# Optimization experiments

Measured on AMD Instinct MI355X. Metric: run time of the kernel, lower is better.

Reference implementation:

```python
import jax, jax.numpy as jnp
import numpy as np

N = 384          # nodes per graph
HID = 128        # hid_dim
H = 8            # shared_num_heads
C = HID // H     # shared_head_dim = 16
L = 4            # num_layers
VOCAB = 20
NORB = 4
NCAT = NORB * NORB + NORB   # 20 edge categories
OUT = 10
B = 4
E = N * N        # fully-connected closure incl. self loops
EPS = 1e-5


def layer_norm(x, g, b):
    m = jnp.mean(x, axis=-1, keepdims=True)
    v = jnp.mean((x - m) ** 2, axis=-1, keepdims=True)
    return (x - m) / jnp.sqrt(v + EPS) * g + b


def setup_inputs() -> dict:
    key = jax.random.key(0)
    ks = iter(jax.random.split(key, 32))

    def nrm(shape, s=0.05):
        return jax.random.normal(next(ks), shape, jnp.float32) * s

    # edge structure: fully connected, edge (i,j) in row-major order
    pos = np.arange(N) % NORB                    # node -> orbit
    src = np.repeat(np.arange(N), N)
    tgt = np.tile(np.arange(N), N)
    cat = np.where(src == tgt, NORB * NORB + pos[src], pos[src] * NORB + pos[tgt])

    x = jax.random.randint(next(ks), (B, N, 1), 0, VOCAB, jnp.int32)

    return dict(
        x=x,
        edge_src=jnp.asarray(src, jnp.int32),
        edge_tgt=jnp.asarray(tgt, jnp.int32),
        edge_cat=jnp.asarray(cat, jnp.int32),
        token_emb=nrm((VOCAB, HID), 1.0),
        edge_emb=nrm((NCAT, HID), 1.0),
        ln_in1_g=jnp.ones((HID,), jnp.float32), ln_in1_b=jnp.zeros((HID,), jnp.float32),
        W_in=nrm((HID, HID)), b_in=jnp.zeros((HID,), jnp.float32),
        ln_in2_g=jnp.ones((HID,), jnp.float32), ln_in2_b=jnp.zeros((HID,), jnp.float32),
        Wl=nrm((L, HID, H * C)), bl=jnp.zeros((L, H * C), jnp.float32),
        Wr=nrm((L, HID, H * C)), br=jnp.zeros((L, H * C), jnp.float32),
        We=nrm((L, HID, H * C)),                           # lin_edge has no bias in PyG GATv2Conv
        att=nrm((L, H, C)),
        bias_gat=jnp.zeros((L, H * C), jnp.float32),
        W_proj=nrm((L, HID, HID)), b_proj=jnp.zeros((L, HID), jnp.float32),
        ln_g=jnp.ones((L, HID), jnp.float32), ln_b=jnp.zeros((L, HID), jnp.float32),
        W_out=nrm((HID, OUT)), b_out=jnp.zeros((OUT,), jnp.float32),
    )


def reference(x, edge_src, edge_tgt, edge_cat,
              token_emb, edge_emb,
              ln_in1_g, ln_in1_b, W_in, b_in, ln_in2_g, ln_in2_b,
              Wl, bl, Wr, br, We, att, bias_gat,
              W_proj, b_proj, ln_g, ln_b, W_out, b_out):
    edge_feat = edge_emb[edge_cat]                       # [E, HID] gather by category
    h = token_emb[x[..., 0]]                             # [B, N, HID]
    # input MLP: LN -> ReLU -> Linear -> LN
    h = layer_norm(h, ln_in1_g, ln_in1_b)
    h = jax.nn.relu(h)
    h = h @ W_in + b_in
    h = layer_norm(h, ln_in2_g, ln_in2_b)

    for l in range(L):
        edge_e = (edge_feat @ We[l]).reshape(E, H, C)    # shared across batch

        def conv(hb):  # hb: [N, HID]  GATv2Conv, concat heads
            xl = (hb @ Wl[l] + bl[l]).reshape(N, H, C)   # source transform
            xr = (hb @ Wr[l] + br[l]).reshape(N, H, C)   # target transform
            e = jax.nn.leaky_relu(xl[edge_src] + xr[edge_tgt] + edge_e, 0.2)  # [E,H,C]
            logits = jnp.einsum('ehc,hc->eh', e, att[l])                      # [E,H]
            # segment softmax over edges sharing a target node
            m = jax.ops.segment_max(logits, edge_tgt, num_segments=N)
            ex = jnp.exp(logits - m[edge_tgt])
            den = jax.ops.segment_sum(ex, edge_tgt, num_segments=N)
            alpha = ex / den[edge_tgt]                                        # [E,H]
            out = jax.ops.segment_sum(xl[edge_src] * alpha[:, :, None], edge_tgt,
                                      num_segments=N)                         # [N,H,C]
            return out.reshape(N, H * C) + bias_gat[l]

        h_prev = h
        h = jax.vmap(conv)(h)                            # [B, N, HID]
        h = h @ W_proj[l] + b_proj[l]
        h = layer_norm(h, ln_g[l], ln_b[l])
        h = jax.nn.relu(h) + h_prev                      # residual

    h = h.sum(axis=1)                                    # sum over nodes -> [B, HID]
    return h @ W_out + b_out                             # [B, OUT]
```

## Files before the change

kernel.cpp:

```cpp
#include <hip/hip_runtime.h>


#define NN 384
#define NB 4
#define TJ 3

__device__ __forceinline__ void reduce32(float& a, float& b) {
#pragma unroll
  for (int m = 1; m <= 16; m <<= 1) {
    a += __shfl_xor(a, m, 64);
    b += __shfl_xor(b, m, 64);
  }
}

__global__ __launch_bounds__(256) void k_init(
    const int* __restrict__ x,
    const float* __restrict__ token_emb, const float* __restrict__ edge_emb,
    const float* __restrict__ ln1g, const float* __restrict__ ln1b,
    const float* __restrict__ W_in, const float* __restrict__ b_in,
    const float* __restrict__ ln2g, const float* __restrict__ ln2b,
    const float* __restrict__ Wl, const float* __restrict__ bl,
    const float* __restrict__ Wr, const float* __restrict__ br,
    const float* __restrict__ We, const float* __restrict__ att_w,
    float* __restrict__ ce, float* __restrict__ h,
    float* __restrict__ xl, float* __restrict__ xr, float* __restrict__ datt0)
{
  const int blk = blockIdx.x, t = threadIdx.x;
  if (blk < 40) {
    const int idx = blk * 256 + t;
    const int hc = idx & 127, rest = idx >> 7;
    const int cat = rest % 20, l = rest / 20;
    const float* er = edge_emb + cat * 128;
    const float* w  = We + (l * 128) * 128 + hc;
    float acc = 0.f;
#pragma unroll 8
    for (int k = 0; k < 128; ++k) acc = fmaf(er[k], w[k * 128], acc);
    ce[idx] = acc;
    return;
  }
  __shared__ float trow[8][128];
  __shared__ float hbuf[8][128];
  const int r0 = (blk - 40) * 8;
  const int r = t >> 5, cw = (t & 31) * 4;
  const int row = r0 + r;
  const int tok = x[row];
  float4 v = *(const float4*)(token_emb + tok * 128 + cw);
  float s1 = v.x + v.y + v.z + v.w;
  float s2 = v.x * v.x + v.y * v.y + v.z * v.z + v.w * v.w;
  reduce32(s1, s2);
  float mean = s1 * 0.0078125f;
  float inv  = rsqrtf(s2 * 0.0078125f - mean * mean + 1e-5f);
  {
    float4 g  = *(const float4*)(ln1g + cw);
    float4 bb = *(const float4*)(ln1b + cw);
    trow[r][cw + 0] = fmaxf((v.x - mean) * inv * g.x + bb.x, 0.f);
    trow[r][cw + 1] = fmaxf((v.y - mean) * inv * g.y + bb.y, 0.f);
    trow[r][cw + 2] = fmaxf((v.z - mean) * inv * g.z + bb.z, 0.f);
    trow[r][cw + 3] = fmaxf((v.w - mean) * inv * g.w + bb.w, 0.f);
  }
  __syncthreads();
  const int o = t & 127, rh = (t >> 7) * 4;
  float a0, a1, a2, a3;
  { float bo = b_in[o]; a0 = a1 = a2 = a3 = bo; }
  for (int k = 0; k < 128; ++k) {
    float w = W_in[k * 128 + o];
    a0 = fmaf(trow[rh + 0][k], w, a0);
    a1 = fmaf(trow[rh + 1][k], w, a1);
    a2 = fmaf(trow[rh + 2][k], w, a2);
    a3 = fmaf(trow[rh + 3][k], w, a3);
  }
  hbuf[rh + 0][o] = a0; hbuf[rh + 1][o] = a1;
  hbuf[rh + 2][o] = a2; hbuf[rh + 3][o] = a3;
  __syncthreads();
  v = *(const float4*)(&hbuf[r][cw]);
  s1 = v.x + v.y + v.z + v.w;
  s2 = v.x * v.x + v.y * v.y + v.z * v.z + v.w * v.w;
  reduce32(s1, s2);
  mean = s1 * 0.0078125f;
  inv  = rsqrtf(s2 * 0.0078125f - mean * mean + 1e-5f);
  {
    float4 g  = *(const float4*)(ln2g + cw);
    float4 bb = *(const float4*)(ln2b + cw);
    float4 hv;
    hv.x = (v.x - mean) * inv * g.x + bb.x;
    hv.y = (v.y - mean) * inv * g.y + bb.y;
    hv.z = (v.z - mean) * inv * g.z + bb.z;
    hv.w = (v.w - mean) * inv * g.w + bb.w;
    *(float4*)(&trow[r][cw]) = hv;
    *(float4*)(h + row * 128 + cw) = hv;
  }
  __syncthreads();
  float l0, l1, l2, l3, q0, q1, q2, q3;
  { float blo = bl[o], bro = br[o]; l0 = l1 = l2 = l3 = blo; q0 = q1 = q2 = q3 = bro; }
  for (int k = 0; k < 128; ++k) {
    float wl = Wl[k * 128 + o], wr = Wr[k * 128 + o];
    float h0 = trow[rh + 0][k], h1 = trow[rh + 1][k];
    float h2 = trow[rh + 2][k], h3 = trow[rh + 3][k];
    l0 = fmaf(h0, wl, l0); q0 = fmaf(h0, wr, q0);
    l1 = fmaf(h1, wl, l1); q1 = fmaf(h1, wr, q1);
    l2 = fmaf(h2, wl, l2); q2 = fmaf(h2, wr, q2);
    l3 = fmaf(h3, wl, l3); q3 = fmaf(h3, wr, q3);
  }
  const int rb = r0 + rh;
  xl[(rb + 0) * 128 + o] = l0; xr[(rb + 0) * 128 + o] = q0;
  xl[(rb + 1) * 128 + o] = l1; xr[(rb + 1) * 128 + o] = q1;
  xl[(rb + 2) * 128 + o] = l2; xr[(rb + 2) * 128 + o] = q2;
  xl[(rb + 3) * 128 + o] = l3; xr[(rb + 3) * 128 + o] = q3;
  {
    float av = att_w[o];
    float s0 = av * l0, sA = av * l1, sB = av * l2, sC = av * l3;
#pragma unroll
    for (int mm = 1; mm <= 8; mm <<= 1) {
      s0 += __shfl_xor(s0, mm, 64);
      sA += __shfl_xor(sA, mm, 64);
      sB += __shfl_xor(sB, mm, 64);
      sC += __shfl_xor(sC, mm, 64);
    }
    if ((t & 15) == 0) {
      const int hh2 = o >> 4;
      const int bb2 = r0 / NN, ii = r0 - bb2 * NN + rh;
      const int base = (bb2 * 8 + hh2) * NN + ii;
      datt0[base + 0] = s0; datt0[base + 1] = sA;
      datt0[base + 2] = sB; datt0[base + 3] = sC;
    }
  }
}

__global__ __launch_bounds__(256) void k_layer(
    const float* __restrict__ xl_in, const float* __restrict__ xr_in,
    const float* __restrict__ datt_in,
    float* __restrict__ xl_out, float* __restrict__ xr_out,
    float* __restrict__ datt_out,
    float* __restrict__ h, const float* __restrict__ ce,
    const float* __restrict__ att_w, const float* __restrict__ bias_gat,
    const float* __restrict__ W_proj, const float* __restrict__ b_proj,
    const float* __restrict__ ln_g, const float* __restrict__ ln_b,
    const float* __restrict__ Wl, const float* __restrict__ bl,
    const float* __restrict__ Wr, const float* __restrict__ br,
    int l, int next_l)
{
  __shared__ float xrce[TJ][5][136];
  __shared__ float djr02[TJ][5][8];
  __shared__ float mbuf[8][32][17];
  __shared__ float arow[TJ][132];
  __shared__ float pbuf[2 * TJ][132];
  __shared__ float nrow[TJ][132];

  const int blk = blockIdx.x, t = threadIdx.x;
  const int jt = blk & 127, b = blk >> 7;
  const int j0 = jt * TJ;

  for (int idx = t; idx < TJ * 5 * 128; idx += 256) {
    const int hc = idx & 127, rest = idx >> 7;
    const int sel = rest % 5, jj = rest / 5;
    const int j = j0 + jj, pj = j & 3;
    const int cat = (sel == 4) ? (16 + pj) : (sel * 4 + pj);
    xrce[jj][sel][hc] = xr_in[(b * NN + j) * 128 + hc] + ce[(l * 20 + cat) * 128 + hc];
  }
  __syncthreads();
  if (t < TJ * 5 * 8) {
    const int jj = t / 40, r2 = t % 40, sel = r2 >> 3, h2 = r2 & 7;
    float d = 0.f;
#pragma unroll
    for (int c = 0; c < 16; ++c)
      d += xrce[jj][sel][h2 * 16 + c] * att_w[l * 128 + h2 * 16 + c];
    djr02[jj][sel][h2] = 0.2f * d;
  }
  __syncthreads();

  const int hh = t >> 5, isub = t & 31;
  float attv[16];
  {
    const float* ap = att_w + l * 128 + hh * 16;
#pragma unroll
    for (int c = 0; c < 16; ++c) attv[c] = ap[c];
  }
  float sden[TJ];
  float acc[TJ][16];
#pragma unroll
  for (int jj = 0; jj < TJ; ++jj) {
    sden[jj] = 0.f;
#pragma unroll
    for (int c = 0; c < 16; ++c) acc[jj][c] = 0.f;
  }
  const float* xlb = xl_in + (b * NN) * 128 + hh * 16;
  const float* dp  = datt_in + (b * 8 + hh) * NN;

  for (int it = 0; it < NN / 32; ++it) {
    const int i = isub + 32 * it;
    float xv[16];
    {
      const float4* xp = (const float4*)(xlb + i * 128);
#pragma unroll
      for (int q = 0; q < 4; ++q) {
        float4 a = xp[q];
        xv[q * 4 + 0] = a.x; xv[q * 4 + 1] = a.y;
        xv[q * 4 + 2] = a.z; xv[q * 4 + 3] = a.w;
      }
    }
    const float di02 = 0.2f * dp[i];
    const int pi = i & 3;
#pragma unroll
    for (int jj = 0; jj < TJ; ++jj) {
      const int sel = (i == j0 + jj) ? 4 : pi;
      const float4* bp = (const float4*)(&xrce[jj][sel][hh * 16]);
      float p = 0.f;
#pragma unroll
      for (int q = 0; q < 4; ++q) {
        float4 cv = bp[q];
        p = fmaf(fmaxf(xv[q * 4 + 0] + cv.x, 0.f), attv[q * 4 + 0], p);
        p = fmaf(fmaxf(xv[q * 4 + 1] + cv.y, 0.f), attv[q * 4 + 1], p);
        p = fmaf(fmaxf(xv[q * 4 + 2] + cv.z, 0.f), attv[q * 4 + 2], p);
        p = fmaf(fmaxf(xv[q * 4 + 3] + cv.w, 0.f), attv[q * 4 + 3], p);
      }
      const float e = __expf(fmaf(0.8f, p, di02 + djr02[jj][sel][hh]));
      sden[jj] += e;
#pragma unroll
      for (int c = 0; c < 16; ++c) acc[jj][c] = fmaf(e, xv[c], acc[jj][c]);
    }
  }

  for (int jj = 0; jj < TJ; ++jj) {
    __syncthreads();
    mbuf[hh][isub][0] = sden[jj];
#pragma unroll
    for (int c = 0; c < 16; ++c) mbuf[hh][isub][1 + c] = acc[jj][c];
    __syncthreads();
    if (t < 128) {
      const int h2 = t >> 4, c2 = t & 15;
      float den = 0.f, num = 0.f;
#pragma unroll 8
      for (int u = 0; u < 32; ++u) {
        den += mbuf[h2][u][0];
        num += mbuf[h2][u][1 + c2];
      }
      arow[jj][t] = num / den + bias_gat[l * 128 + t];
    }
  }
  __syncthreads();

  {
    const int o = t & 127, half = t >> 7;
    const float* Wp = W_proj + l * 16384;
    float p0 = 0.f, p1 = 0.f, p2 = 0.f;
    const int k0 = half * 64;
    for (int kk = 0; kk < 64; ++kk) {
      const int k = k0 + kk;
      const float w = Wp[k * 128 + o];
      p0 = fmaf(arow[0][k], w, p0);
      p1 = fmaf(arow[1][k], w, p1);
      p2 = fmaf(arow[2][k], w, p2);
    }
    pbuf[half * 3 + 0][o] = p0;
    pbuf[half * 3 + 1][o] = p1;
    pbuf[half * 3 + 2][o] = p2;
  }
  __syncthreads();
  if (t < 128) {
    const float bo = b_proj[l * 128 + t];
    nrow[0][t] = pbuf[0][t] + pbuf[3][t] + bo;
    nrow[1][t] = pbuf[1][t] + pbuf[4][t] + bo;
    nrow[2][t] = pbuf[2][t] + pbuf[5][t] + bo;
  }
  __syncthreads();

  {
    const int w = t >> 6;
    if (w < TJ) {
      const int c2 = (t & 63) * 2;
      float v0 = nrow[w][c2], v1 = nrow[w][c2 + 1];
      float s1 = v0 + v1, s2 = v0 * v0 + v1 * v1;
#pragma unroll
      for (int m = 1; m <= 32; m <<= 1) {
        s1 += __shfl_xor(s1, m, 64);
        s2 += __shfl_xor(s2, m, 64);
      }
      const float mean = s1 * 0.0078125f;
      const float inv  = rsqrtf(s2 * 0.0078125f - mean * mean + 1e-5f);
      const int row = (b * NN + j0 + w) * 128;
      const float g0 = ln_g[l * 128 + c2], g1 = ln_g[l * 128 + c2 + 1];
      const float b0 = ln_b[l * 128 + c2], b1 = ln_b[l * 128 + c2 + 1];
      const float hp0 = h[row + c2], hp1 = h[row + c2 + 1];
      const float hn0 = fmaxf((v0 - mean) * inv * g0 + b0, 0.f) + hp0;
      const float hn1 = fmaxf((v1 - mean) * inv * g1 + b1, 0.f) + hp1;
      h[row + c2] = hn0; h[row + c2 + 1] = hn1;
      nrow[w][c2] = hn0; nrow[w][c2 + 1] = hn1;
    }
  }
  __syncthreads();

  if (next_l >= 0) {
    const int o = t & 127, m = t >> 7;
    const float* W = (m ? Wr : Wl) + next_l * 16384;
    const float bias = (m ? br : bl)[next_l * 128 + o];
    float a0 = bias, a1 = bias, a2 = bias;
    for (int k = 0; k < 128; ++k) {
      const float wv = W[k * 128 + o];
      a0 = fmaf(nrow[0][k], wv, a0);
      a1 = fmaf(nrow[1][k], wv, a1);
      a2 = fmaf(nrow[2][k], wv, a2);
    }
    float* dst = m ? xr_out : xl_out;
    const int rb = (b * NN + j0) * 128 + o;
    dst[rb] = a0; dst[rb + 128] = a1; dst[rb + 256] = a2;
    if (m == 0) {
      const float av = att_w[next_l * 128 + o];
      float s0 = av * a0, s1 = av * a1, s2 = av * a2;
#pragma unroll
      for (int mm = 1; mm <= 8; mm <<= 1) {
        s0 += __shfl_xor(s0, mm, 64);
        s1 += __shfl_xor(s1, mm, 64);
        s2 += __shfl_xor(s2, mm, 64);
      }
      if ((t & 15) == 0) {
        const int base = (b * 8 + (o >> 4)) * NN + j0;
        datt_out[base + 0] = s0;
        datt_out[base + 1] = s1;
        datt_out[base + 2] = s2;
      }
    }
  }
}

__global__ __launch_bounds__(256) void k_final(
    const float* __restrict__ h, const float* __restrict__ W_out,
    const float* __restrict__ b_out, float* __restrict__ out)
{
  __shared__ float sbuf[2][128];
  const int bq = blockIdx.x, t = threadIdx.x;
  const int o = t & 127, half = t >> 7;
  float acc = 0.f;
  const float* hp = h + (bq * NN + half * 192) * 128 + o;
  for (int n = 0; n < 192; ++n) acc += hp[n * 128];
  sbuf[half][o] = acc;
  __syncthreads();
  if (t < 10) {
    float a = b_out[t];
#pragma unroll 8
    for (int k = 0; k < 128; ++k)
      a = fmaf(sbuf[0][k] + sbuf[1][k], W_out[k * 10 + t], a);
    out[bq * 10 + t] = a;
  }
}

extern "C" void kernel_launch(void* const* d_in, const int* in_sizes, int n_in,
                              void* d_out, int out_size, void* d_ws, size_t ws_size,
                              hipStream_t stream) {
  const int*   x         = (const int*)d_in[0];
  const float* token_emb = (const float*)d_in[4];
  const float* edge_emb  = (const float*)d_in[5];
  const float* ln1g      = (const float*)d_in[6];
  const float* ln1b      = (const float*)d_in[7];
  const float* W_in      = (const float*)d_in[8];
  const float* b_in      = (const float*)d_in[9];
  const float* ln2g      = (const float*)d_in[10];
  const float* ln2b      = (const float*)d_in[11];
  const float* Wl        = (const float*)d_in[12];
  const float* bl        = (const float*)d_in[13];
  const float* Wr        = (const float*)d_in[14];
  const float* br        = (const float*)d_in[15];
  const float* We        = (const float*)d_in[16];
  const float* att_w     = (const float*)d_in[17];
  const float* bias_gat  = (const float*)d_in[18];
  const float* W_proj    = (const float*)d_in[19];
  const float* b_proj    = (const float*)d_in[20];
  const float* ln_g      = (const float*)d_in[21];
  const float* ln_b      = (const float*)d_in[22];
  const float* W_out     = (const float*)d_in[23];
  const float* b_out     = (const float*)d_in[24];

  float* ws  = (float*)d_ws;
  float* ce  = ws;
  float* h   = ce  + 10240;
  float* xlA = h   + 196608;
  float* xrA = xlA + 196608;
  float* xlB = xrA + 196608;
  float* xrB = xlB + 196608;
  float* dA  = xrB + 196608;
  float* dB  = dA  + 12288;

  k_init<<<dim3(40 + 192), 256, 0, stream>>>(
      x, token_emb, edge_emb, ln1g, ln1b, W_in, b_in, ln2g, ln2b,
      Wl, bl, Wr, br, We, att_w, ce, h, xlA, xrA, dA);
  for (int l = 0; l < 4; ++l) {
    const bool even = (l & 1) == 0;
    float* xin  = even ? xlA : xlB;  float* rin  = even ? xrA : xrB;
    float* din  = even ? dA  : dB;
    float* xout = even ? xlB : xlA;  float* rout = even ? xrB : xrA;
    float* dout = even ? dB  : dA;
    k_layer<<<dim3(NB * (NN / TJ)), 256, 0, stream>>>(
        xin, rin, din, xout, rout, dout, h, ce, att_w, bias_gat,
        W_proj, b_proj, ln_g, ln_b, Wl, bl, Wr, br, l, (l < 3) ? l + 1 : -1);
  }
  k_final<<<dim3(NB), 256, 0, stream>>>(h, W_out, b_out, (float*)d_out);
}
```

Baseline: 230.5 us.

## Fuse all stages into one persistent kernel with software grid barriers

Merges the init, four layer and final kernels into a single persistent launch of 512 blocks. Stages are separated by atomic-counter grid barriers whose counters are zeroed by a memset before launch. Init work is redistributed so that each block computes its own rows' embedding, LayerNorm and input projection, plus a slice of the edge-category table. This removes kernel launch gaps and tail effects, at the cost of barrier spin overhead and a reliance on all 512 blocks being co-resident, which launch_bounds(256,2) is meant to help ensure.

```diff
diff --git a/kernel.cpp b/kernel.cpp
--- a/kernel.cpp
+++ b/kernel.cpp
@@ -4,249 +4,82 @@
 #define NN 384
 #define NB 4
 #define TJ 3
-
-__device__ __forceinline__ void reduce32(float& a, float& b) {
-#pragma unroll
-  for (int m = 1; m <= 16; m <<= 1) {
-    a += __shfl_xor(a, m, 64);
-    b += __shfl_xor(b, m, 64);
-  }
+#define GRID 512
+
+struct Params {
+  const int* x;
+  const float *token_emb, *edge_emb;
+  const float *ln1g, *ln1b, *W_in, *b_in, *ln2g, *ln2b;
+  const float *Wl, *bl, *Wr, *br, *We, *att_w, *bias_gat;
+  const float *W_proj, *b_proj, *ln_g, *ln_b, *W_out, *b_out;
+  unsigned* bar;
+  float *ce, *h, *xlA, *xrA, *xlB, *xrB, *dA, *dB, *out;
+};
+
+__device__ __forceinline__ void gbar(unsigned* cnt) {
+  __syncthreads();
+  if (threadIdx.x == 0) {
+    __threadfence();
+    __hip_atomic_fetch_add(cnt, 1u, __ATOMIC_RELEASE, __HIP_MEMORY_SCOPE_AGENT);
+    while (__hip_atomic_load(cnt, __ATOMIC_ACQUIRE, __HIP_MEMORY_SCOPE_AGENT) < GRID)
+      __builtin_amdgcn_s_sleep(1);
+    __threadfence();
+  }
+  __syncthreads();
 }
 
-__global__ __launch_bounds__(256) void k_init(
-    const int* __restrict__ x,
-    const float* __restrict__ token_emb, const float* __restrict__ edge_emb,
-    const float* __restrict__ ln1g, const float* __restrict__ ln1b,
-    const float* __restrict__ W_in, const float* __restrict__ b_in,
-    const float* __restrict__ ln2g, const float* __restrict__ ln2b,
-    const float* __restrict__ Wl, const float* __restrict__ bl,
-    const float* __restrict__ Wr, const float* __restrict__ br,
-    const float* __restrict__ We, const float* __restrict__ att_w,
-    float* __restrict__ ce, float* __restrict__ h,
-    float* __restrict__ xl, float* __restrict__ xr, float* __restrict__ datt0)
-{
-  const int blk = blockIdx.x, t = threadIdx.x;
-  if (blk < 40) {
-    const int idx = blk * 256 + t;
-    const int hc = idx & 127, rest = idx >> 7;
-    const int cat = rest % 20, l = rest / 20;
-    const float* er = edge_emb + cat * 128;
-    const float* w  = We + (l * 128) * 128 + hc;
-    float acc = 0.f;
-#pragma unroll 8
-    for (int k = 0; k < 128; ++k) acc = fmaf(er[k], w[k * 128], acc);
-    ce[idx] = acc;
-    return;
-  }
-  __shared__ float trow[8][128];
-  __shared__ float hbuf[8][128];
-  const int r0 = (blk - 40) * 8;
-  const int r = t >> 5, cw = (t & 31) * 4;
-  const int row = r0 + r;
-  const int tok = x[row];
-  float4 v = *(const float4*)(token_emb + tok * 128 + cw);
-  float s1 = v.x + v.y + v.z + v.w;
-  float s2 = v.x * v.x + v.y * v.y + v.z * v.z + v.w * v.w;
-  reduce32(s1, s2);
-  float mean = s1 * 0.0078125f;
-  float inv  = rsqrtf(s2 * 0.0078125f - mean * mean + 1e-5f);
-  {
-    float4 g  = *(const float4*)(ln1g + cw);
-    float4 bb = *(const float4*)(ln1b + cw);
-    trow[r][cw + 0] = fmaxf((v.x - mean) * inv * g.x + bb.x, 0.f);
-    trow[r][cw + 1] = fmaxf((v.y - mean) * inv * g.y + bb.y, 0.f);
-    trow[r][cw + 2] = fmaxf((v.z - mean) * inv * g.z + bb.z, 0.f);
-    trow[r][cw + 3] = fmaxf((v.w - mean) * inv * g.w + bb.w, 0.f);
-  }
-  __syncthreads();
-  const int o = t & 127, rh = (t >> 7) * 4;
-  float a0, a1, a2, a3;
-  { float bo = b_in[o]; a0 = a1 = a2 = a3 = bo; }
-  for (int k = 0; k < 128; ++k) {
-    float w = W_in[k * 128 + o];
-    a0 = fmaf(trow[rh + 0][k], w, a0);
-    a1 = fmaf(trow[rh + 1][k], w, a1);
-    a2 = fmaf(trow[rh + 2][k], w, a2);
-    a3 = fmaf(trow[rh + 3][k], w, a3);
-  }
-  hbuf[rh + 0][o] = a0; hbuf[rh + 1][o] = a1;
-  hbuf[rh + 2][o] = a2; hbuf[rh + 3][o] = a3;
-  __syncthreads();
-  v = *(const float4*)(&hbuf[r][cw]);
-  s1 = v.x + v.y + v.z + v.w;
-  s2 = v.x * v.x + v.y * v.y + v.z * v.z + v.w * v.w;
-  reduce32(s1, s2);
-  mean = s1 * 0.0078125f;
-  inv  = rsqrtf(s2 * 0.0078125f - mean * mean + 1e-5f);
-  {
-    float4 g  = *(const float4*)(ln2g + cw);
-    float4 bb = *(const float4*)(ln2b + cw);
-    float4 hv;
-    hv.x = (v.x - mean) * inv * g.x + bb.x;
-    hv.y = (v.y - mean) * inv * g.y + bb.y;
-    hv.z = (v.z - mean) * inv * g.z + bb.z;
-    hv.w = (v.w - mean) * inv * g.w + bb.w;
-    *(float4*)(&trow[r][cw]) = hv;
-    *(float4*)(h + row * 128 + cw) = hv;
-  }
-  __syncthreads();
-  float l0, l1, l2, l3, q0, q1, q2, q3;
-  { float blo = bl[o], bro = br[o]; l0 = l1 = l2 = l3 = blo; q0 = q1 = q2 = q3 = bro; }
-  for (int k = 0; k < 128; ++k) {
-    float wl = Wl[k * 128 + o], wr = Wr[k * 128 + o];
-    float h0 = trow[rh + 0][k], h1 = trow[rh + 1][k];
-    float h2 = trow[rh + 2][k], h3 = trow[rh + 3][k];
-    l0 = fmaf(h0, wl, l0); q0 = fmaf(h0, wr, q0);
-    l1 = fmaf(h1, wl, l1); q1 = fmaf(h1, wr, q1);
-    l2 = fmaf(h2, wl, l2); q2 = fmaf(h2, wr, q2);
-    l3 = fmaf(h3, wl, l3); q3 = fmaf(h3, wr, q3);
-  }
-  const int rb = r0 + rh;
-  xl[(rb + 0) * 128 + o] = l0; xr[(rb + 0) * 128 + o] = q0;
-  xl[(rb + 1) * 128 + o] = l1; xr[(rb + 1) * 128 + o] = q1;
-  xl[(rb + 2) * 128 + o] = l2; xr[(rb + 2) * 128 + o] = q2;
-  xl[(rb + 3) * 128 + o] = l3; xr[(rb + 3) * 128 + o] = q3;
-  {
-    float av = att_w[o];
-    float s0 = av * l0, sA = av * l1, sB = av * l2, sC = av * l3;
-#pragma unroll
-    for (int mm = 1; mm <= 8; mm <<= 1) {
-      s0 += __shfl_xor(s0, mm, 64);
-      sA += __shfl_xor(sA, mm, 64);
-      sB += __shfl_xor(sB, mm, 64);
-      sC += __shfl_xor(sC, mm, 64);
-    }
-    if ((t & 15) == 0) {
-      const int hh2 = o >> 4;
-      const int bb2 = r0 / NN, ii = r0 - bb2 * NN + rh;
-      const int base = (bb2 * 8 + hh2) * NN + ii;
-      datt0[base + 0] = s0; datt0[base + 1] = sA;
-      datt0[base + 2] = sB; datt0[base + 3] = sC;
-    }
-  }
-}
-
-__global__ __launch_bounds__(256) void k_layer(
-    const float* __restrict__ xl_in, const float* __restrict__ xr_in,
-    const float* __restrict__ datt_in,
-    float* __restrict__ xl_out, float* __restrict__ xr_out,
-    float* __restrict__ datt_out,
-    float* __restrict__ h, const float* __restrict__ ce,
-    const float* __restrict__ att_w, const float* __restrict__ bias_gat,
-    const float* __restrict__ W_proj, const float* __restrict__ b_proj,
-    const float* __restrict__ ln_g, const float* __restrict__ ln_b,
-    const float* __restrict__ Wl, const float* __restrict__ bl,
-    const float* __restrict__ Wr, const float* __restrict__ br,
-    int l, int next_l)
-{
+__global__ __launch_bounds__(256, 2) void k_all(Params P) {
   __shared__ float xrce[TJ][5][136];
-  __shared__ float djr02[TJ][5][8];
-  __shared__ float mbuf[8][32][17];
+  __shared__ float djr02s[TJ][5][8];
+  __shared__ float mbuf[8][545];
   __shared__ float arow[TJ][132];
   __shared__ float pbuf[2 * TJ][132];
   __shared__ float nrow[TJ][132];
 
   const int blk = blockIdx.x, t = threadIdx.x;
-  const int jt = blk & 127, b = blk >> 7;
-  const int j0 = jt * TJ;
-
-  for (int idx = t; idx < TJ * 5 * 128; idx += 256) {
-    const int hc = idx & 127, rest = idx >> 7;
-    const int sel = rest % 5, jj = rest / 5;
-    const int j = j0 + jj, pj = j & 3;
-    const int cat = (sel == 4) ? (16 + pj) : (sel * 4 + pj);
-    xrce[jj][sel][hc] = xr_in[(b * NN + j) * 128 + hc] + ce[(l * 20 + cat) * 128 + hc];
-  }
-  __syncthreads();
-  if (t < TJ * 5 * 8) {
-    const int jj = t / 40, r2 = t % 40, sel = r2 >> 3, h2 = r2 & 7;
-    float d = 0.f;
-#pragma unroll
-    for (int c = 0; c < 16; ++c)
-      d += xrce[jj][sel][h2 * 16 + c] * att_w[l * 128 + h2 * 16 + c];
-    djr02[jj][sel][h2] = 0.2f * d;
-  }
-  __syncthreads();
-
-  const int hh = t >> 5, isub = t & 31;
-  float attv[16];
+  const int b = blk >> 7, jt = blk & 127, j0 = jt * TJ;
+  const int gr0 = b * NN + j0;
+
+  if (t < 160) {
+    const int gidx = blk * 20 + (t >> 3), s = t & 7;
+    const int hc = gidx & 127, rest = gidx >> 7;
+    const int cat = rest % 20, l = rest / 20;
+    const float* er = P.edge_emb + cat * 128 + s * 16;
+    const float* w  = P.We + l * 16384 + (s * 16) * 128 + hc;
+    float acc = 0.f;
+#pragma unroll
+    for (int k = 0; k < 16; ++k) acc = fmaf(er[k], w[k * 128], acc);
+    acc += __shfl_xor(acc, 1, 64);
+    acc += __shfl_xor(acc, 2, 64);
+    acc += __shfl_xor(acc, 4, 64);
+    if (s == 0) P.ce[gidx] = acc;
+  }
   {
-    const float* ap = att_w + l * 128 + hh * 16;
-#pragma unroll
-    for (int c = 0; c < 16; ++c) attv[c] = ap[c];
-  }
-  float sden[TJ];
-  float acc[TJ][16];
-#pragma unroll
-  for (int jj = 0; jj < TJ; ++jj) {
-    sden[jj] = 0.f;
-#pragma unroll
-    for (int c = 0; c < 16; ++c) acc[jj][c] = 0.f;
-  }
-  const float* xlb = xl_in + (b * NN) * 128 + hh * 16;
-  const float* dp  = datt_in + (b * 8 + hh) * NN;
-
-  for (int it = 0; it < NN / 32; ++it) {
-    const int i = isub + 32 * it;
-    float xv[16];
-    {
-      const float4* xp = (const float4*)(xlb + i * 128);
-#pragma unroll
-      for (int q = 0; q < 4; ++q) {
-        float4 a = xp[q];
-        xv[q * 4 + 0] = a.x; xv[q * 4 + 1] = a.y;
-        xv[q * 4 + 2] = a.z; xv[q * 4 + 3] = a.w;
-      }
-    }
-    const float di02 = 0.2f * dp[i];
-    const int pi = i & 3;
-#pragma unroll
-    for (int jj = 0; jj < TJ; ++jj) {
-      const int sel = (i == j0 + jj) ? 4 : pi;
-      const float4* bp = (const float4*)(&xrce[jj][sel][hh * 16]);
-      float p = 0.f;
-#pragma unroll
-      for (int q = 0; q < 4; ++q) {
-        float4 cv = bp[q];
-        p = fmaf(fmaxf(xv[q * 4 + 0] + cv.x, 0.f), attv[q * 4 + 0], p);
-        p = fmaf(fmaxf(xv[q * 4 + 1] + cv.y, 0.f), attv[q * 4 + 1], p);
-        p = fmaf(fmaxf(xv[q * 4 + 2] + cv.z, 0.f), attv[q * 4 + 2], p);
-        p = fmaf(fmaxf(xv[q * 4 + 3] + cv.w, 0.f), attv[q * 4 + 3], p);
-      }
-      const float e = __expf(fmaf(0.8f, p, di02 + djr02[jj][sel][hh]));
-      sden[jj] += e;
-#pragma unroll
-      for (int c = 0; c < 16; ++c) acc[jj][c] = fmaf(e, xv[c], acc[jj][c]);
-    }
-  }
-
-  for (int jj = 0; jj < TJ; ++jj) {
-    __syncthreads();
-    mbuf[hh][isub][0] = sden[jj];
-#pragma unroll
-    for (int c = 0; c < 16; ++c) mbuf[hh][isub][1 + c] = acc[jj][c];
-    __syncthreads();
-    if (t < 128) {
-      const int h2 = t >> 4, c2 = t & 15;
-      float den = 0.f, num = 0.f;
-#pragma unroll 8
-      for (int u = 0; u < 32; ++u) {
-        den += mbuf[h2][u][0];
-        num += mbuf[h2][u][1 + c2];
-      }
-      arow[jj][t] = num / den + bias_gat[l * 128 + t];
-    }
-  }
-  __syncthreads();
-
+    const int w = t >> 6;
+    if (w < TJ) {
+      const int c2 = (t & 63) * 2;
+      const int tok = P.x[gr0 + w];
+      const float* te = P.token_emb + tok * 128;
+      float v0 = te[c2], v1 = te[c2 + 1];
+      float s1 = v0 + v1, s2 = v0 * v0 + v1 * v1;
+#pragma unroll
+      for (int m = 1; m <= 32; m <<= 1) {
+        s1 += __shfl_xor(s1, m, 64);
+        s2 += __shfl_xor(s2, m, 64);
+      }
+      const float mean = s1 * 0.0078125f;
+      const float inv  = rsqrtf(s2 * 0.0078125f - mean * mean + 1e-5f);
+      arow[w][c2]     = fmaxf((v0 - mean) * inv * P.ln1g[c2]     + P.ln1b[c2],     0.f);
+      arow[w][c2 + 1] = fmaxf((v1 - mean) * inv * P.ln1g[c2 + 1] + P.ln1b[c2 + 1], 0.f);
+    }
+  }
+  __syncthreads();
   {
-    const int o = t & 127, half = t >> 7;
-    const float* Wp = W_proj + l * 16384;
+    const int o = t & 127, half = t >> 7, k0 = half * 64;
     float p0 = 0.f, p1 = 0.f, p2 = 0.f;
-    const int k0 = half * 64;
     for (int kk = 0; kk < 64; ++kk) {
       const int k = k0 + kk;
-      const float w = Wp[k * 128 + o];
+      const float w = P.W_in[k * 128 + o];
       p0 = fmaf(arow[0][k], w, p0);
       p1 = fmaf(arow[1][k], w, p1);
       p2 = fmaf(arow[2][k], w, p2);
@@ -257,13 +90,12 @@
   }
   __syncthreads();
   if (t < 128) {
-    const float bo = b_proj[l * 128 + t];
+    const float bo = P.b_in[t];
     nrow[0][t] = pbuf[0][t] + pbuf[3][t] + bo;
     nrow[1][t] = pbuf[1][t] + pbuf[4][t] + bo;
     nrow[2][t] = pbuf[2][t] + pbuf[5][t] + bo;
   }
   __syncthreads();
-
   {
     const int w = t >> 6;
     if (w < TJ) {
@@ -277,22 +109,18 @@
       }
       const float mean = s1 * 0.0078125f;
       const float inv  = rsqrtf(s2 * 0.0078125f - mean * mean + 1e-5f);
-      const int row = (b * NN + j0 + w) * 128;
-      const float g0 = ln_g[l * 128 + c2], g1 = ln_g[l * 128 + c2 + 1];
-      const float b0 = ln_b[l * 128 + c2], b1 = ln_b[l * 128 + c2 + 1];
-      const float hp0 = h[row + c2], hp1 = h[row + c2 + 1];
-      const float hn0 = fmaxf((v0 - mean) * inv * g0 + b0, 0.f) + hp0;
-      const float hn1 = fmaxf((v1 - mean) * inv * g1 + b1, 0.f) + hp1;
-      h[row + c2] = hn0; h[row + c2 + 1] = hn1;
+      const float hn0 = (v0 - mean) * inv * P.ln2g[c2]     + P.ln2b[c2];
+      const float hn1 = (v1 - mean) * inv * P.ln2g[c2 + 1] + P.ln2b[c2 + 1];
+      const int row = (gr0 + w) * 128;
+      P.h[row + c2] = hn0; P.h[row + c2 + 1] = hn1;
       nrow[w][c2] = hn0; nrow[w][c2 + 1] = hn1;
     }
   }
   __syncthreads();
-
-  if (next_l >= 0) {
+  {
     const int o = t & 127, m = t >> 7;
-    const float* W = (m ? Wr : Wl) + next_l * 16384;
-    const float bias = (m ? br : bl)[next_l * 128 + o];
+    const float* W = (m ? P.Wr : P.Wl);
+    const float bias = (m ? P.br : P.bl)[o];
     float a0 = bias, a1 = bias, a2 = bias;
     for (int k = 0; k < 128; ++k) {
       const float wv = W[k * 128 + o];
@@ -300,11 +128,11 @@
       a1 = fmaf(nrow[1][k], wv, a1);
       a2 = fmaf(nrow[2][k], wv, a2);
     }
-    float* dst = m ? xr_out : xl_out;
-    const int rb = (b * NN + j0) * 128 + o;
+    float* dst = m ? P.xrA : P.xlA;
+    const int rb = gr0 * 128 + o;
     dst[rb] = a0; dst[rb + 128] = a1; dst[rb + 256] = a2;
     if (m == 0) {
-      const float av = att_w[next_l * 128 + o];
+      const float av = P.att_w[o];
       float s0 = av * a0, s1 = av * a1, s2 = av * a2;
 #pragma unroll
       for (int mm = 1; mm <= 8; mm <<= 1) {
@@ -314,83 +142,250 @@
       }
       if ((t & 15) == 0) {
         const int base = (b * 8 + (o >> 4)) * NN + j0;
-        datt_out[base + 0] = s0;
-        datt_out[base + 1] = s1;
-        datt_out[base + 2] = s2;
-      }
-    }
-  }
-}
-
-__global__ __launch_bounds__(256) void k_final(
-    const float* __restrict__ h, const float* __restrict__ W_out,
-    const float* __restrict__ b_out, float* __restrict__ out)
-{
-  __shared__ float sbuf[2][128];
-  const int bq = blockIdx.x, t = threadIdx.x;
-  const int o = t & 127, half = t >> 7;
-  float acc = 0.f;
-  const float* hp = h + (bq * NN + half * 192) * 128 + o;
-  for (int n = 0; n < 192; ++n) acc += hp[n * 128];
-  sbuf[half][o] = acc;
-  __syncthreads();
-  if (t < 10) {
-    float a = b_out[t];
+        P.dA[base] = s0; P.dA[base + 1] = s1; P.dA[base + 2] = s2;
+      }
+    }
+  }
+  gbar(P.bar + 0);
+
+  float *xin = P.xlA, *rin = P.xrA, *din = P.dA;
+  float *xout = P.xlB, *rout = P.xrB, *dout = P.dB;
+
+  for (int l = 0; l < 4; ++l) {
+    for (int idx = t; idx < TJ * 5 * 128; idx += 256) {
+      const int hc = idx & 127, rest = idx >> 7;
+      const int sel = rest % 5, jj = rest / 5;
+      const int j = j0 + jj, pj = j & 3;
+      const int cat = (sel == 4) ? (16 + pj) : (sel * 4 + pj);
+      xrce[jj][sel][hc] = rin[(b * NN + j) * 128 + hc] + P.ce[(l * 20 + cat) * 128 + hc];
+    }
+    __syncthreads();
+    if (t < TJ * 5 * 8) {
+      const int jj = t / 40, r2 = t % 40, sel = r2 >> 3, h2 = r2 & 7;
+      float d = 0.f;
+#pragma unroll
+      for (int c = 0; c < 16; ++c)
+        d += xrce[jj][sel][h2 * 16 + c] * P.att_w[l * 128 + h2 * 16 + c];
+      djr02s[jj][sel][h2] = 0.2f * d;
+    }
+    __syncthreads();
+
+    const int hh = t >> 5, isub = t & 31;
+    float attv[16];
+    {
+      const float* ap = P.att_w + l * 128 + hh * 16;
+#pragma unroll
+      for (int c = 0; c < 16; ++c) attv[c] = ap[c];
+    }
+    float sden[TJ];
+    float acc[TJ][16];
+#pragma unroll
+    for (int jj = 0; jj < TJ; ++jj) {
+      sden[jj] = 0.f;
+#pragma unroll
+      for (int c = 0; c < 16; ++c) acc[jj][c] = 0.f;
+    }
+    const float* xlb = xin + (b * NN) * 128 + hh * 16;
+    const float* dp  = din + (b * 8 + hh) * NN;
+
+    for (int it = 0; it < NN / 32; ++it) {
+      const int i = isub + 32 * it;
+      float xv[16];
+      {
+        const float4* xp = (const float4*)(xlb + i * 128);
+#pragma unroll
+        for (int q = 0; q < 4; ++q) {
+          float4 a = xp[q];
+          xv[q * 4 + 0] = a.x; xv[q * 4 + 1] = a.y;
+          xv[q * 4 + 2] = a.z; xv[q * 4 + 3] = a.w;
+        }
+      }
+      const float di02 = 0.2f * dp[i];
+      const int pi = i & 3;
+#pragma unroll
+      for (int jj = 0; jj < TJ; ++jj) {
+        const int sel = (i == j0 + jj) ? 4 : pi;
+        const float4* bp = (const float4*)(&xrce[jj][sel][hh * 16]);
+        float p = 0.f;
+#pragma unroll
+        for (int q = 0; q < 4; ++q) {
+          float4 cv = bp[q];
+          p = fmaf(fmaxf(xv[q * 4 + 0] + cv.x, 0.f), attv[q * 4 + 0], p);
+          p = fmaf(fmaxf(xv[q * 4 + 1] + cv.y, 0.f), attv[q * 4 + 1], p);
+          p = fmaf(fmaxf(xv[q * 4 + 2] + cv.z, 0.f), attv[q * 4 + 2], p);
+          p = fmaf(fmaxf(xv[q * 4 + 3] + cv.w, 0.f), attv[q * 4 + 3], p);
+        }
+        const float e = __expf(fmaf(0.8f, p, di02 + djr02s[jj][sel][hh]));
+        sden[jj] += e;
+#pragma unroll
+        for (int c = 0; c < 16; ++c) acc[jj][c] = fmaf(e, xv[c], acc[jj][c]);
+      }
+    }
+
+    for (int jj = 0; jj < TJ; ++jj) {
+      __syncthreads();
+      mbuf[hh][isub * 17] = sden[jj];
+#pragma unroll
+      for (int c = 0; c < 16; ++c) mbuf[hh][isub * 17 + 1 + c] = acc[jj][c];
+      __syncthreads();
+      if (t < 128) {
+        const int h2 = t >> 4, c2 = t & 15;
+        float den = 0.f, num = 0.f;
 #pragma unroll 8
-    for (int k = 0; k < 128; ++k)
-      a = fmaf(sbuf[0][k] + sbuf[1][k], W_out[k * 10 + t], a);
-    out[bq * 10 + t] = a;
+        for (int u = 0; u < 32; ++u) {
+          den += mbuf[h2][u * 17];
+          num += mbuf[h2][u * 17 + 1 + c2];
+        }
+        arow[jj][t] = num / den + P.bias_gat[l * 128 + t];
+      }
+    }
+    __syncthreads();
+
+    {
+      const int o = t & 127, half = t >> 7, k0 = half * 64;
+      const float* Wp = P.W_proj + l * 16384;
+      float p0 = 0.f, p1 = 0.f, p2 = 0.f;
+      for (int kk = 0; kk < 64; ++kk) {
+        const int k = k0 + kk;
+        const float w = Wp[k * 128 + o];
+        p0 = fmaf(arow[0][k], w, p0);
+        p1 = fmaf(arow[1][k], w, p1);
+        p2 = fmaf(arow[2][k], w, p2);
+      }
+      pbuf[half * 3 + 0][o] = p0;
+      pbuf[half * 3 + 1][o] = p1;
+      pbuf[half * 3 + 2][o] = p2;
+    }
+    __syncthreads();
+    if (t < 128) {
+      const float bo = P.b_proj[l * 128 + t];
+      nrow[0][t] = pbuf[0][t] + pbuf[3][t] + bo;
+      nrow[1][t] = pbuf[1][t] + pbuf[4][t] + bo;
+      nrow[2][t] = pbuf[2][t] + pbuf[5][t] + bo;
+    }
+    __syncthreads();
+
+    {
+      const int w = t >> 6;
+      if (w < TJ) {
+        const int c2 = (t & 63) * 2;
+        float v0 = nrow[w][c2], v1 = nrow[w][c2 + 1];
+        float s1 = v0 + v1, s2 = v0 * v0 + v1 * v1;
+#pragma unroll
+        for (int m = 1; m <= 32; m <<= 1) {
+          s1 += __shfl_xor(s1, m, 64);
+          s2 += __shfl_xor(s2, m, 64);
+        }
+        const float mean = s1 * 0.0078125f;
+        const float inv  = rsqrtf(s2 * 0.0078125f - mean * mean + 1e-5f);
+        const int row = (gr0 + w) * 128;
+        const float g0 = P.ln_g[l * 128 + c2], g1 = P.ln_g[l * 128 + c2 + 1];
+        const float b0 = P.ln_b[l * 128 + c2], b1 = P.ln_b[l * 128 + c2 + 1];
+        const float hp0 = P.h[row + c2], hp1 = P.h[row + c2 + 1];
+        const float hn0 = fmaxf((v0 - mean) * inv * g0 + b0, 0.f) + hp0;
+        const float hn1 = fmaxf((v1 - mean) * inv * g1 + b1, 0.f) + hp1;
+        P.h[row + c2] = hn0; P.h[row + c2 + 1] = hn1;
+        nrow[w][c2] = hn0; nrow[w][c2 + 1] = hn1;
+      }
+    }
+    __syncthreads();
+
+    if (l < 3) {
+      const int nl = l + 1;
+      const int o = t & 127, m = t >> 7;
+      const float* W = (m ? P.Wr : P.Wl) + nl * 16384;
+      const float bias = (m ? P.br : P.bl)[nl * 128 + o];
+      float a0 = bias, a1 = bias, a2 = bias;
+      for (int k = 0; k < 128; ++k) {
+        const float wv = W[k * 128 + o];
+        a0 = fmaf(nrow[0][k], wv, a0);
+        a1 = fmaf(nrow[1][k], wv, a1);
+        a2 = fmaf(nrow[2][k], wv, a2);
+      }
+      float* dst = m ? rout : xout;
+      const int rb = gr0 * 128 + o;
+      dst[rb] = a0; dst[rb + 128] = a1; dst[rb + 256] = a2;
+      if (m == 0) {
+        const float av = P.att_w[nl * 128 + o];
+        float s0 = av * a0, s1 = av * a1, s2 = av * a2;
+#pragma unroll
+        for (int mm = 1; mm <= 8; mm <<= 1) {
+          s0 += __shfl_xor(s0, mm, 64);
+          s1 += __shfl_xor(s1, mm, 64);
+          s2 += __shfl_xor(s2, mm, 64);
+        }
+        if ((t & 15) == 0) {
+          const int base = (b * 8 + (o >> 4)) * NN + j0;
+          dout[base] = s0; dout[base + 1] = s1; dout[base + 2] = s2;
+        }
+      }
+    }
+    gbar(P.bar + 1 + l);
+    float* tmp;
+    tmp = xin; xin = xout; xout = tmp;
+    tmp = rin; rin = rout; rout = tmp;
+    tmp = din; din = dout; dout = tmp;
+  }
+
+  if (blk < NB) {
+    const int o = t & 127, half = t >> 7;
+    float acc0 = 0.f, acc1 = 0.f;
+    const float* hp = P.h + (blk * NN + half * 192) * 128 + o;
+    for (int n = 0; n < 96; ++n) {
+      acc0 += hp[(2 * n) * 128];
+      acc1 += hp[(2 * n + 1) * 128];
+    }
+    pbuf[half][o] = acc0 + acc1;
+    __syncthreads();
+    if (t < 10) {
+      float a = P.b_out[t];
+#pragma unroll 8
+      for (int k = 0; k < 128; ++k)
+        a = fmaf(pbuf[0][k] + pbuf[1][k], P.W_out[k * 10 + t], a);
+      P.out[blk * 10 + t] = a;
+    }
   }
 }
 
 extern "C" void kernel_launch(void* const* d_in, const int* in_sizes, int n_in,
                               void* d_out, int out_size, void* d_ws, size_t ws_size,
                               hipStream_t stream) {
-  const int*   x         = (const int*)d_in[0];
-  const float* token_emb = (const float*)d_in[4];
-  const float* edge_emb  = (const float*)d_in[5];
-  const float* ln1g      = (const float*)d_in[6];
-  const float* ln1b      = (const float*)d_in[7];
-  const float* W_in      = (const float*)d_in[8];
-  const float* b_in      = (const float*)d_in[9];
-  const float* ln2g      = (const float*)d_in[10];
-  const float* ln2b      = (const float*)d_in[11];
-  const float* Wl        = (const float*)d_in[12];
-  const float* bl        = (const float*)d_in[13];
-  const float* Wr        = (const float*)d_in[14];
-  const float* br        = (const float*)d_in[15];
-  const float* We        = (const float*)d_in[16];
-  const float* att_w     = (const float*)d_in[17];
-  const float* bias_gat  = (const float*)d_in[18];
-  const float* W_proj    = (const float*)d_in[19];
-  const float* b_proj    = (const float*)d_in[20];
-  const float* ln_g      = (const float*)d_in[21];
-  const float* ln_b      = (const float*)d_in[22];
-  const float* W_out     = (const float*)d_in[23];
-  const float* b_out     = (const float*)d_in[24];
-
-  float* ws  = (float*)d_ws;
-  float* ce  = ws;
-  float* h   = ce  + 10240;
-  float* xlA = h   + 196608;
-  float* xrA = xlA + 196608;
-  float* xlB = xrA + 196608;
-  float* xrB = xlB + 196608;
-  float* dA  = xrB + 196608;
-  float* dB  = dA  + 12288;
-
-  k_init<<<dim3(40 + 192), 256, 0, stream>>>(
-      x, token_emb, edge_emb, ln1g, ln1b, W_in, b_in, ln2g, ln2b,
-      Wl, bl, Wr, br, We, att_w, ce, h, xlA, xrA, dA);
-  for (int l = 0; l < 4; ++l) {
-    const bool even = (l & 1) == 0;
-    float* xin  = even ? xlA : xlB;  float* rin  = even ? xrA : xrB;
-    float* din  = even ? dA  : dB;
-    float* xout = even ? xlB : xlA;  float* rout = even ? xrB : xrA;
-    float* dout = even ? dB  : dA;
-    k_layer<<<dim3(NB * (NN / TJ)), 256, 0, stream>>>(
-        xin, rin, din, xout, rout, dout, h, ce, att_w, bias_gat,
-        W_proj, b_proj, ln_g, ln_b, Wl, bl, Wr, br, l, (l < 3) ? l + 1 : -1);
-  }
-  k_final<<<dim3(NB), 256, 0, stream>>>(h, W_out, b_out, (float*)d_out);
+  Params P;
+  P.x         = (const int*)d_in[0];
+  P.token_emb = (const float*)d_in[4];
+  P.edge_emb  = (const float*)d_in[5];
+  P.ln1g      = (const float*)d_in[6];
+  P.ln1b      = (const float*)d_in[7];
+  P.W_in      = (const float*)d_in[8];
+  P.b_in      = (const float*)d_in[9];
+  P.ln2g      = (const float*)d_in[10];
+  P.ln2b      = (const float*)d_in[11];
+  P.Wl        = (const float*)d_in[12];
+  P.bl        = (const float*)d_in[13];
+  P.Wr        = (const float*)d_in[14];
+  P.br        = (const float*)d_in[15];
+  P.We        = (const float*)d_in[16];
+  P.att_w     = (const float*)d_in[17];
+  P.bias_gat  = (const float*)d_in[18];
+  P.W_proj    = (const float*)d_in[19];
+  P.b_proj    = (const float*)d_in[20];
+  P.ln_g      = (const float*)d_in[21];
+  P.ln_b      = (const float*)d_in[22];
+  P.W_out     = (const float*)d_in[23];
+  P.b_out     = (const float*)d_in[24];
+
+  float* ws = (float*)d_ws;
+  P.bar = (unsigned*)d_ws;
+  P.ce  = ws + 64;
+  P.h   = P.ce  + 10240;
+  P.xlA = P.h   + 196608;
+  P.xrA = P.xlA + 196608;
+  P.xlB = P.xrA + 196608;
+  P.xrB = P.xlB + 196608;
+  P.dA  = P.xrB + 196608;
+  P.dB  = P.dA  + 12288;
+  P.out = (float*)d_out;
+
+  hipMemsetAsync(d_ws, 0, 256, stream);
+  k_all<<<dim3(GRID), dim3(256), 0, stream>>>(P);
 }
```

Result: slower. 525.9 us (+128.1%).
